# Performance work log

Hardware: AMD Instinct MI355X
Metric: run time of the kernel (lower is better)

The kernel has to match this reference:

```python
import jax, jax.numpy as jnp
import numpy as np

B, SQ, SKV, D = 8, 2048, 2048, 1024

def setup_inputs() -> dict:
    key = jax.random.key(0)
    ks = jax.random.split(key, 8)
    s = 1.0 / np.sqrt(D)  # torch Linear default init range
    return {
        "target": jax.random.normal(ks[0], (B, SQ, D), dtype=jnp.float32),
        "non_target": jax.random.normal(ks[1], (B, SKV, D), dtype=jnp.float32),
        "Wq": jax.random.uniform(ks[2], (D, D), jnp.float32, -s, s),
        "bq": jax.random.uniform(ks[3], (D,), jnp.float32, -s, s),
        "Wk": jax.random.uniform(ks[4], (D, D), jnp.float32, -s, s),
        "bk": jax.random.uniform(ks[5], (D,), jnp.float32, -s, s),
        "Wv": jax.random.uniform(ks[6], (D, D), jnp.float32, -s, s),
        "bv": jax.random.uniform(ks[7], (D,), jnp.float32, -s, s),
    }

def reference(target, non_target, Wq, bq, Wk, bk, Wv, bv):
    # Linear projections (torch Linear: x @ W.T + b)
    q = jnp.einsum('bsd,ed->bse', target, Wq) + bq       # [B,SQ,D]
    k = jnp.einsum('bsd,ed->bse', non_target, Wk) + bk   # [B,SKV,D]
    v = jnp.einsum('bsd,ed->bse', non_target, Wv) + bv   # [B,SKV,D]
    # Unscaled attention, exactly as the original module (no 1/sqrt(d))
    scores = jnp.einsum('bqd,bkd->bqk', q, k)            # [B,SQ,SKV]
    weights = jax.nn.softmax(scores, axis=-1)
    return jnp.einsum('bqk,bkd->bqd', weights, v)        # [B,SQ,D]
```

## Files before the change

kernel.cpp:

```cpp
#include <hip/hip_runtime.h>


typedef _Float16 half8 __attribute__((ext_vector_type(8)));
typedef _Float16 half4v __attribute__((ext_vector_type(4)));
typedef float floatx4 __attribute__((ext_vector_type(4)));

__device__ __forceinline__ void async_copy16(const _Float16* g, _Float16* l) {
  __builtin_amdgcn_global_load_lds(
      (const __attribute__((address_space(1))) void*)g,
      (__attribute__((address_space(3))) void*)l,
      16, 0, 0);
}

__global__ __launch_bounds__(256) void cast_f32_f16(const float* __restrict__ src,
                                                    _Float16* __restrict__ dst, long n) {
  long i = ((long)blockIdx.x * 256 + threadIdx.x) * 8;
  if (i >= n) return;
  float4 a = *(const float4*)(src + i);
  float4 b = *(const float4*)(src + i + 4);
  half8 h;
  h[0] = (_Float16)a.x; h[1] = (_Float16)a.y; h[2] = (_Float16)a.z; h[3] = (_Float16)a.w;
  h[4] = (_Float16)b.x; h[5] = (_Float16)b.y; h[6] = (_Float16)b.z; h[7] = (_Float16)b.w;
  *(half8*)(dst + i) = h;
}

template <int OMODE>
__global__ __launch_bounds__(256, 2) void gemm_bt(const _Float16* __restrict__ A,
                                                  const _Float16* __restrict__ B,
                                                  const float* __restrict__ bias,
                                                  void* __restrict__ out,
                                                  int K, int N,
                                                  long sA, long sB, long sO) {
  __shared__ __attribute__((aligned(16))) _Float16 As[128 * 64];
  __shared__ __attribute__((aligned(16))) _Float16 Bs[128 * 64];

  const int tid = threadIdx.x;
  const int lane = tid & 63;
  const int wave = tid >> 6;
  const long bz = blockIdx.z;

  const _Float16* Ab = A + bz * sA + (long)blockIdx.x * 128 * K;
  const _Float16* Bb = B + bz * sB + (long)blockIdx.y * 128 * K;

  const int wm = (wave & 1) * 64;
  const int wn = (wave >> 1) * 64;
  const int frow = lane & 15;
  const int fq = lane >> 4;
  const int fsw = frow & 7;

  floatx4 acc[4][4];
#pragma unroll
  for (int mt = 0; mt < 4; mt++)
#pragma unroll
    for (int nt = 0; nt < 4; nt++)
      acc[mt][nt] = (floatx4){0.f, 0.f, 0.f, 0.f};

  const int sr = tid >> 3;
  const int gl = (tid & 7) ^ (sr & 7);
  const long gOffBase = (long)sr * K + gl * 8;
  const int ldsOff = tid * 8;

  for (int k0 = 0; k0 < K; k0 += 64) {
    __syncthreads();
#pragma unroll
    for (int j = 0; j < 4; j++) {
      async_copy16(Ab + gOffBase + (long)(32 * j) * K + k0, As + ldsOff + j * 2048);
      async_copy16(Bb + gOffBase + (long)(32 * j) * K + k0, Bs + ldsOff + j * 2048);
    }
    __syncthreads();

#pragma unroll
    for (int h = 0; h < 2; h++) {
      half8 af[4], bf[4];
#pragma unroll
      for (int mt = 0; mt < 4; mt++)
        af[mt] = *(const half8*)(As + (wm + mt * 16 + frow) * 64 + ((h * 4 + fq) ^ fsw) * 8);
#pragma unroll
      for (int nt = 0; nt < 4; nt++)
        bf[nt] = *(const half8*)(Bs + (wn + nt * 16 + frow) * 64 + ((h * 4 + fq) ^ fsw) * 8);
#pragma unroll
      for (int mt = 0; mt < 4; mt++)
#pragma unroll
        for (int nt = 0; nt < 4; nt++)
          acc[mt][nt] = __builtin_amdgcn_mfma_f32_16x16x32_f16(af[mt], bf[nt], acc[mt][nt], 0, 0, 0);
    }
  }

  if (OMODE == 2 || OMODE == 3) {
#pragma unroll
    for (int nt = 0; nt < 4; nt++) {
      const int n = blockIdx.y * 128 + wn + nt * 16 + frow;
#pragma unroll
      for (int mt = 0; mt < 4; mt++) {
        const int rbase = blockIdx.x * 128 + wm + mt * 16 + fq * 4;
#pragma unroll
        for (int i = 0; i < 4; i++) {
          if (OMODE == 2)
            ((float*)out + bz * sO)[(long)(rbase + i) * N + n] = acc[mt][nt][i];
          else
            ((_Float16*)out + bz * sO)[(long)(rbase + i) * N + n] = (_Float16)acc[mt][nt][i];
        }
      }
    }
  } else {
#pragma unroll
    for (int nt = 0; nt < 4; nt++) {
      const int n = blockIdx.y * 128 + wn + nt * 16 + frow;
      const float bvv = bias[n];
#pragma unroll
      for (int mt = 0; mt < 4; mt++) {
        const int rbase = blockIdx.x * 128 + wm + mt * 16 + fq * 4;
        if (OMODE == 0) {
#pragma unroll
          for (int i = 0; i < 4; i++)
            ((_Float16*)out)[(long)(rbase + i) * N + n] = (_Float16)(acc[mt][nt][i] + bvv);
        } else {
          const long bb = rbase >> 11;
          const int s = rbase & 2047;
          half4v hv;
#pragma unroll
          for (int i = 0; i < 4; i++) hv[i] = (_Float16)(acc[mt][nt][i] + bvv);
          *(half4v*)((_Float16*)out + bb * (2048l * 1024) + (long)n * 2048 + s) = hv;
        }
      }
    }
  }
}

__global__ __launch_bounds__(256) void softmax_rows(const _Float16* __restrict__ S,
                                                    _Float16* __restrict__ P) {
  const long row = blockIdx.x;
  const _Float16* src = S + row * 2048;
  _Float16* dst = P + row * 2048;
  const int tid = threadIdx.x;

  half8 v = ((const half8*)src)[tid];
  float f[8];
#pragma unroll
  for (int i = 0; i < 8; i++) f[i] = (float)v[i];

  float m = fmaxf(fmaxf(fmaxf(f[0], f[1]), fmaxf(f[2], f[3])),
                  fmaxf(fmaxf(f[4], f[5]), fmaxf(f[6], f[7])));
#pragma unroll
  for (int o = 32; o > 0; o >>= 1) m = fmaxf(m, __shfl_xor(m, o, 64));
  __shared__ float redm[4];
  if ((tid & 63) == 0) redm[tid >> 6] = m;
  __syncthreads();
  m = fmaxf(fmaxf(redm[0], redm[1]), fmaxf(redm[2], redm[3]));

  float e[8], s = 0.f;
#pragma unroll
  for (int i = 0; i < 8; i++) { e[i] = __expf(f[i] - m); s += e[i]; }
#pragma unroll
  for (int o = 32; o > 0; o >>= 1) s += __shfl_xor(s, o, 64);
  __shared__ float reds[4];
  if ((tid & 63) == 0) reds[tid >> 6] = s;
  __syncthreads();
  s = (reds[0] + reds[1]) + (reds[2] + reds[3]);
  const float inv = 1.f / s;

  half8 h;
#pragma unroll
  for (int i = 0; i < 8; i++) h[i] = (_Float16)(e[i] * inv);
  ((half8*)dst)[tid] = h;
}

extern "C" void kernel_launch(void* const* d_in, const int* in_sizes, int n_in,
                              void* d_out, int out_size, void* d_ws, size_t ws_size,
                              hipStream_t stream) {
  const float* target = (const float*)d_in[0];
  const float* non_target = (const float*)d_in[1];
  const float* Wq = (const float*)d_in[2];
  const float* bq = (const float*)d_in[3];
  const float* Wk = (const float*)d_in[4];
  const float* bk = (const float*)d_in[5];
  const float* Wv = (const float*)d_in[6];
  const float* bv = (const float*)d_in[7];

  char* ws = (char*)d_ws;
  const size_t MB = 1ull << 20;
  _Float16* tgt16 = (_Float16*)(ws);
  _Float16* ntg16 = (_Float16*)(ws + 32 * MB);
  _Float16* S16 = (_Float16*)(ws);
  _Float16* P16 = (_Float16*)(ws + 64 * MB);
  _Float16* Q16 = (_Float16*)(ws + 128 * MB);
  _Float16* K16 = (_Float16*)(ws + 160 * MB);
  _Float16* Vt16 = (_Float16*)(ws + 192 * MB);
  _Float16* Wq16 = (_Float16*)(ws + 224 * MB);
  _Float16* Wk16 = (_Float16*)(ws + 226 * MB);
  _Float16* Wv16 = (_Float16*)(ws + 228 * MB);

  const long nBig = 8l * 2048 * 1024;
  const long nW = 1024l * 1024;

  cast_f32_f16<<<8192, 256, 0, stream>>>(target, tgt16, nBig);
  cast_f32_f16<<<8192, 256, 0, stream>>>(non_target, ntg16, nBig);
  cast_f32_f16<<<512, 256, 0, stream>>>(Wq, Wq16, nW);
  cast_f32_f16<<<512, 256, 0, stream>>>(Wk, Wk16, nW);
  cast_f32_f16<<<512, 256, 0, stream>>>(Wv, Wv16, nW);

  gemm_bt<0><<<dim3(128, 8, 1), 256, 0, stream>>>(tgt16, Wq16, bq, Q16, 1024, 1024, 0, 0, 0);
  gemm_bt<0><<<dim3(128, 8, 1), 256, 0, stream>>>(ntg16, Wk16, bk, K16, 1024, 1024, 0, 0, 0);
  gemm_bt<1><<<dim3(128, 8, 1), 256, 0, stream>>>(ntg16, Wv16, bv, Vt16, 1024, 1024, 0, 0, 0);

  gemm_bt<3><<<dim3(16, 16, 8), 256, 0, stream>>>(Q16, K16, nullptr, S16, 1024, 2048,
                                                  2048l * 1024, 2048l * 1024, 2048l * 2048);

  softmax_rows<<<16384, 256, 0, stream>>>(S16, P16);

  gemm_bt<2><<<dim3(16, 8, 8), 256, 0, stream>>>(P16, Vt16, nullptr, (float*)d_out, 2048, 1024,
                                                 2048l * 2048, 1024l * 2048, 2048l * 1024);
}
```

Measured before the change: 479.0 us.

## Replace 128x128 GEMM with 256x256 tile, 4-stage async LDS pipeline

Replaces the GEMM kernel with a 512-thread, 256x256-tile version. It uses a 4-slot ring of 32-wide K chunks in LDS, prefetches three chunks ahead with global_load_lds, and interleaves the A/B prefetches with MFMA phases. Barriers are split, with s_setprio raised around the MFMA blocks. The aim is to hide global load latency and raise arithmetic intensity per block. In exchange it uses 128KB of LDS per block and launches fewer blocks, which can cut occupancy or leave CUs idle on the smaller GEMMs.

Measured after the change: 495.3 us. 3.4% more time.

```diff
diff --git a/kernel.cpp b/kernel.cpp
--- a/kernel.cpp
+++ b/kernel.cpp
@@ -25,102 +25,139 @@
 }
 
 template <int OMODE>
-__global__ __launch_bounds__(256, 2) void gemm_bt(const _Float16* __restrict__ A,
-                                                  const _Float16* __restrict__ B,
+__global__ __launch_bounds__(512, 2) void gemm256(const _Float16* __restrict__ A,
+                                                  const _Float16* __restrict__ Bm,
                                                   const float* __restrict__ bias,
                                                   void* __restrict__ out,
                                                   int K, int N,
                                                   long sA, long sB, long sO) {
-  __shared__ __attribute__((aligned(16))) _Float16 As[128 * 64];
-  __shared__ __attribute__((aligned(16))) _Float16 Bs[128 * 64];
+  __shared__ __attribute__((aligned(16))) _Float16 lds[65536];
+  _Float16* Ar = lds;
+  _Float16* Br = lds + 32768;
 
   const int tid = threadIdx.x;
   const int lane = tid & 63;
   const int wave = tid >> 6;
+  const int wm = wave >> 2;
+  const int wn = wave & 3;
+  const int frow = lane & 15;
+  const int fq = (lane >> 4) & 3;
   const long bz = blockIdx.z;
 
-  const _Float16* Ab = A + bz * sA + (long)blockIdx.x * 128 * K;
-  const _Float16* Bb = B + bz * sB + (long)blockIdx.y * 128 * K;
-
-  const int wm = (wave & 1) * 64;
-  const int wn = (wave >> 1) * 64;
-  const int frow = lane & 15;
-  const int fq = lane >> 4;
-  const int fsw = frow & 7;
-
-  floatx4 acc[4][4];
-#pragma unroll
-  for (int mt = 0; mt < 4; mt++)
-#pragma unroll
-    for (int nt = 0; nt < 4; nt++)
-      acc[mt][nt] = (floatx4){0.f, 0.f, 0.f, 0.f};
-
-  const int sr = tid >> 3;
-  const int gl = (tid & 7) ^ (sr & 7);
-  const long gOffBase = (long)sr * K + gl * 8;
-  const int ldsOff = tid * 8;
-
-  for (int k0 = 0; k0 < K; k0 += 64) {
-    __syncthreads();
-#pragma unroll
-    for (int j = 0; j < 4; j++) {
-      async_copy16(Ab + gOffBase + (long)(32 * j) * K + k0, As + ldsOff + j * 2048);
-      async_copy16(Bb + gOffBase + (long)(32 * j) * K + k0, Bs + ldsOff + j * 2048);
-    }
-    __syncthreads();
-
-#pragma unroll
-    for (int h = 0; h < 2; h++) {
-      half8 af[4], bf[4];
-#pragma unroll
-      for (int mt = 0; mt < 4; mt++)
-        af[mt] = *(const half8*)(As + (wm + mt * 16 + frow) * 64 + ((h * 4 + fq) ^ fsw) * 8);
-#pragma unroll
-      for (int nt = 0; nt < 4; nt++)
-        bf[nt] = *(const half8*)(Bs + (wn + nt * 16 + frow) * 64 + ((h * 4 + fq) ^ fsw) * 8);
-#pragma unroll
-      for (int mt = 0; mt < 4; mt++)
-#pragma unroll
-        for (int nt = 0; nt < 4; nt++)
-          acc[mt][nt] = __builtin_amdgcn_mfma_f32_16x16x32_f16(af[mt], bf[nt], acc[mt][nt], 0, 0, 0);
-    }
+  const _Float16* Ab = A + bz * sA + (long)blockIdx.x * 256 * K;
+  const _Float16* Bb = Bm + bz * sB + (long)blockIdx.y * 256 * K;
+
+  const int glog = (tid & 7) ^ ((tid >> 3) & 7);
+  const long sg = (long)(2 * (tid >> 3) + (glog >> 2)) * K + (glog & 3) * 8;
+  const int ldst = tid * 8;
+  const long lK128 = (long)K * 128;
+
+  const int gphys = ((frow & 1) * 4 + fq) ^ (frow >> 1);
+  const int aoff = (frow >> 1) * 64 + gphys * 8;
+
+  floatx4 acc[8][4];
+#pragma unroll
+  for (int m = 0; m < 8; ++m)
+#pragma unroll
+    for (int n = 0; n < 4; ++n) acc[m][n] = (floatx4){0.f, 0.f, 0.f, 0.f};
+
+  const int NK = K >> 5;
+
+#pragma unroll
+  for (int kp = 0; kp < 3; ++kp) {
+#pragma unroll
+    for (int j = 0; j < 2; ++j)
+      async_copy16(Ab + sg + kp * 32 + j * lK128, Ar + kp * 8192 + ldst + j * 4096);
+#pragma unroll
+    for (int j = 0; j < 2; ++j)
+      async_copy16(Bb + sg + kp * 32 + j * lK128, Br + kp * 8192 + ldst + j * 4096);
   }
-
-  if (OMODE == 2 || OMODE == 3) {
-#pragma unroll
-    for (int nt = 0; nt < 4; nt++) {
-      const int n = blockIdx.y * 128 + wn + nt * 16 + frow;
-#pragma unroll
-      for (int mt = 0; mt < 4; mt++) {
-        const int rbase = blockIdx.x * 128 + wm + mt * 16 + fq * 4;
-#pragma unroll
-        for (int i = 0; i < 4; i++) {
-          if (OMODE == 2)
-            ((float*)out + bz * sO)[(long)(rbase + i) * N + n] = acc[mt][nt][i];
-          else
-            ((_Float16*)out + bz * sO)[(long)(rbase + i) * N + n] = (_Float16)acc[mt][nt][i];
+  asm volatile("s_waitcnt vmcnt(8)" ::: "memory");
+  __builtin_amdgcn_s_barrier();
+
+  for (int kc = 0; kc < NK; ++kc) {
+    const int slot = kc & 3;
+    int ks = kc + 3;
+    if (ks > NK - 1) ks = NK - 1;
+    const int ssl = ks & 3;
+    const _Float16* as = Ar + slot * 8192 + wm * 4096 + aoff;
+    const _Float16* bs = Br + slot * 8192 + wn * 2048 + aoff;
+
+    half8 af[4], bf[4];
+
+#pragma unroll
+    for (int i = 0; i < 4; ++i) af[i] = *(const half8*)(as + i * 512);
+#pragma unroll
+    for (int n = 0; n < 4; ++n) bf[n] = *(const half8*)(bs + n * 512);
+#pragma unroll
+    for (int j = 0; j < 2; ++j)
+      async_copy16(Ab + sg + ks * 32 + j * lK128, Ar + ssl * 8192 + ldst + j * 4096);
+    __builtin_amdgcn_s_barrier();
+    asm volatile("s_waitcnt lgkmcnt(0)" ::: "memory");
+    __builtin_amdgcn_sched_barrier(0);
+    __builtin_amdgcn_s_setprio(1);
+#pragma unroll
+    for (int i = 0; i < 4; ++i)
+#pragma unroll
+      for (int n = 0; n < 4; ++n)
+        acc[i][n] = __builtin_amdgcn_mfma_f32_16x16x32_f16(af[i], bf[n], acc[i][n], 0, 0, 0);
+    __builtin_amdgcn_s_setprio(0);
+    __builtin_amdgcn_s_barrier();
+
+#pragma unroll
+    for (int i = 0; i < 4; ++i) af[i] = *(const half8*)(as + 2048 + i * 512);
+#pragma unroll
+    for (int j = 0; j < 2; ++j)
+      async_copy16(Bb + sg + ks * 32 + j * lK128, Br + ssl * 8192 + ldst + j * 4096);
+    __builtin_amdgcn_s_barrier();
+    asm volatile("s_waitcnt lgkmcnt(0)" ::: "memory");
+    __builtin_amdgcn_sched_barrier(0);
+    __builtin_amdgcn_s_setprio(1);
+#pragma unroll
+    for (int i = 0; i < 4; ++i)
+#pragma unroll
+      for (int n = 0; n < 4; ++n)
+        acc[4 + i][n] = __builtin_amdgcn_mfma_f32_16x16x32_f16(af[i], bf[n], acc[4 + i][n], 0, 0, 0);
+    __builtin_amdgcn_s_setprio(0);
+    asm volatile("s_waitcnt vmcnt(8)" ::: "memory");
+    __builtin_amdgcn_s_barrier();
+  }
+
+  if (OMODE == 0 || OMODE == 1) {
+#pragma unroll
+    for (int n = 0; n < 4; ++n) {
+      const int cg = blockIdx.y * 256 + wn * 64 + n * 16 + frow;
+      const float bvv = bias[cg];
+#pragma unroll
+      for (int m = 0; m < 8; ++m) {
+        const int rg = blockIdx.x * 256 + wm * 128 + m * 16 + fq * 4;
+        if (OMODE == 0) {
+#pragma unroll
+          for (int i = 0; i < 4; ++i)
+            ((_Float16*)out)[(long)(rg + i) * N + cg] = (_Float16)(acc[m][n][i] + bvv);
+        } else {
+          const long bb = rg >> 11;
+          const int s = rg & 2047;
+          half4v hv;
+#pragma unroll
+          for (int i = 0; i < 4; ++i) hv[i] = (_Float16)(acc[m][n][i] + bvv);
+          *(half4v*)((_Float16*)out + bb * (2048l * 1024) + (long)cg * 2048 + s) = hv;
         }
       }
     }
   } else {
 #pragma unroll
-    for (int nt = 0; nt < 4; nt++) {
-      const int n = blockIdx.y * 128 + wn + nt * 16 + frow;
-      const float bvv = bias[n];
-#pragma unroll
-      for (int mt = 0; mt < 4; mt++) {
-        const int rbase = blockIdx.x * 128 + wm + mt * 16 + fq * 4;
-        if (OMODE == 0) {
-#pragma unroll
-          for (int i = 0; i < 4; i++)
-            ((_Float16*)out)[(long)(rbase + i) * N + n] = (_Float16)(acc[mt][nt][i] + bvv);
-        } else {
-          const long bb = rbase >> 11;
-          const int s = rbase & 2047;
-          half4v hv;
-#pragma unroll
-          for (int i = 0; i < 4; i++) hv[i] = (_Float16)(acc[mt][nt][i] + bvv);
-          *(half4v*)((_Float16*)out + bb * (2048l * 1024) + (long)n * 2048 + s) = hv;
+    for (int n = 0; n < 4; ++n) {
+      const int cg = blockIdx.y * 256 + wn * 64 + n * 16 + frow;
+#pragma unroll
+      for (int m = 0; m < 8; ++m) {
+        const int rgl = blockIdx.x * 256 + wm * 128 + m * 16 + fq * 4;
+#pragma unroll
+        for (int i = 0; i < 4; ++i) {
+          if (OMODE == 2)
+            ((float*)out + bz * sO)[(long)(rgl + i) * N + cg] = acc[m][n][i];
+          else
+            ((_Float16*)out + bz * sO)[(long)(rgl + i) * N + cg] = (_Float16)acc[m][n][i];
         }
       }
     }
@@ -199,15 +236,15 @@
   cast_f32_f16<<<512, 256, 0, stream>>>(Wk, Wk16, nW);
   cast_f32_f16<<<512, 256, 0, stream>>>(Wv, Wv16, nW);
 
-  gemm_bt<0><<<dim3(128, 8, 1), 256, 0, stream>>>(tgt16, Wq16, bq, Q16, 1024, 1024, 0, 0, 0);
-  gemm_bt<0><<<dim3(128, 8, 1), 256, 0, stream>>>(ntg16, Wk16, bk, K16, 1024, 1024, 0, 0, 0);
-  gemm_bt<1><<<dim3(128, 8, 1), 256, 0, stream>>>(ntg16, Wv16, bv, Vt16, 1024, 1024, 0, 0, 0);
-
-  gemm_bt<3><<<dim3(16, 16, 8), 256, 0, stream>>>(Q16, K16, nullptr, S16, 1024, 2048,
-                                                  2048l * 1024, 2048l * 1024, 2048l * 2048);
+  gemm256<0><<<dim3(64, 4, 1), 512, 0, stream>>>(tgt16, Wq16, bq, Q16, 1024, 1024, 0, 0, 0);
+  gemm256<0><<<dim3(64, 4, 1), 512, 0, stream>>>(ntg16, Wk16, bk, K16, 1024, 1024, 0, 0, 0);
+  gemm256<1><<<dim3(64, 4, 1), 512, 0, stream>>>(ntg16, Wv16, bv, Vt16, 1024, 1024, 0, 0, 0);
+
+  gemm256<3><<<dim3(8, 8, 8), 512, 0, stream>>>(Q16, K16, nullptr, S16, 1024, 2048,
+                                                2048l * 1024, 2048l * 1024, 2048l * 2048);
 
   softmax_rows<<<16384, 256, 0, stream>>>(S16, P16);
 
-  gemm_bt<2><<<dim3(16, 8, 8), 256, 0, stream>>>(P16, Vt16, nullptr, (float*)d_out, 2048, 1024,
-                                                 2048l * 2048, 1024l * 2048, 2048l * 1024);
-}
+  gemm256<2><<<dim3(8, 4, 8), 512, 0, stream>>>(P16, Vt16, nullptr, (float*)d_out, 2048, 1024,
+                                                2048l * 2048, 1024l * 2048, 2048l * 1024);
+}
```

## Fuse input casts into projection GEMMs and softmax normalization into PV GEMM

Applied to the files above, without the earlier changes.

The projection GEMMs now read fp32 activations directly and convert them to fp16 in registers before the LDS store, so the two large standalone cast kernels and their intermediate buffers go away. The softmax kernel now writes only each row's max and inverse sum, and the PV GEMM applies exp and normalization to the raw scores while loading its A tile, so the probability matrix is never written or read back. The cost is synchronous global loads instead of async LDS copies for the A operand, and exp work repeated for every N-tile block (8 per row block) in the PV GEMM.

Result: slower. 550.4 us (+14.9%).

```diff
diff --git a/kernel.cpp b/kernel.cpp
--- a/kernel.cpp
+++ b/kernel.cpp
@@ -24,10 +24,12 @@
   *(half8*)(dst + i) = h;
 }
 
-template <int OMODE>
-__global__ __launch_bounds__(256, 2) void gemm_bt(const _Float16* __restrict__ A,
+template <int OMODE, int ATRANS>
+__global__ __launch_bounds__(256, 2) void gemm_bt(const void* __restrict__ A,
                                                   const _Float16* __restrict__ B,
                                                   const float* __restrict__ bias,
+                                                  const float* __restrict__ rowM,
+                                                  const float* __restrict__ rowS,
                                                   void* __restrict__ out,
                                                   int K, int N,
                                                   long sA, long sB, long sO) {
@@ -39,7 +41,9 @@
   const int wave = tid >> 6;
   const long bz = blockIdx.z;
 
-  const _Float16* Ab = A + bz * sA + (long)blockIdx.x * 128 * K;
+  const long abase = bz * sA + (long)blockIdx.x * 128 * K;
+  const _Float16* Ah = (const _Float16*)A + abase;
+  const float* Af = (const float*)A + abase;
   const _Float16* Bb = B + bz * sB + (long)blockIdx.y * 128 * K;
 
   const int wm = (wave & 1) * 64;
@@ -60,12 +64,63 @@
   const long gOffBase = (long)sr * K + gl * 8;
   const int ldsOff = tid * 8;
 
+  float mA0 = 0.f, sA0 = 0.f, mA1 = 0.f, sA1 = 0.f;
+  float mA2 = 0.f, sA2 = 0.f, mA3 = 0.f, sA3 = 0.f;
+  if (ATRANS == 2) {
+    const long gr = bz * 2048 + (long)blockIdx.x * 128 + sr;
+    mA0 = rowM[gr];      sA0 = rowS[gr];
+    mA1 = rowM[gr + 32]; sA1 = rowS[gr + 32];
+    mA2 = rowM[gr + 64]; sA2 = rowS[gr + 64];
+    mA3 = rowM[gr + 96]; sA3 = rowS[gr + 96];
+  }
+
   for (int k0 = 0; k0 < K; k0 += 64) {
     __syncthreads();
-#pragma unroll
-    for (int j = 0; j < 4; j++) {
-      async_copy16(Ab + gOffBase + (long)(32 * j) * K + k0, As + ldsOff + j * 2048);
-      async_copy16(Bb + gOffBase + (long)(32 * j) * K + k0, Bs + ldsOff + j * 2048);
+    if (ATRANS == 0) {
+#pragma unroll
+      for (int j = 0; j < 4; j++) {
+        async_copy16(Ah + gOffBase + (long)(32 * j) * K + k0, As + ldsOff + j * 2048);
+        async_copy16(Bb + gOffBase + (long)(32 * j) * K + k0, Bs + ldsOff + j * 2048);
+      }
+    } else if (ATRANS == 1) {
+      floatx4 f0[4], f1[4];
+#pragma unroll
+      for (int j = 0; j < 4; j++) {
+        const float* src = Af + gOffBase + (long)(32 * j) * K + k0;
+        f0[j] = *(const floatx4*)(src);
+        f1[j] = *(const floatx4*)(src + 4);
+      }
+#pragma unroll
+      for (int j = 0; j < 4; j++)
+        async_copy16(Bb + gOffBase + (long)(32 * j) * K + k0, Bs + ldsOff + j * 2048);
+#pragma unroll
+      for (int j = 0; j < 4; j++) {
+        half8 w;
+#pragma unroll
+        for (int t = 0; t < 4; t++) {
+          w[t] = (_Float16)f0[j][t];
+          w[4 + t] = (_Float16)f1[j][t];
+        }
+        *(half8*)(As + ldsOff + j * 2048) = w;
+      }
+    } else {
+      half8 hv[4];
+#pragma unroll
+      for (int j = 0; j < 4; j++)
+        hv[j] = *(const half8*)(Ah + gOffBase + (long)(32 * j) * K + k0);
+#pragma unroll
+      for (int j = 0; j < 4; j++)
+        async_copy16(Bb + gOffBase + (long)(32 * j) * K + k0, Bs + ldsOff + j * 2048);
+#pragma unroll
+      for (int j = 0; j < 4; j++) {
+        const float mj = (j == 0) ? mA0 : (j == 1) ? mA1 : (j == 2) ? mA2 : mA3;
+        const float sj = (j == 0) ? sA0 : (j == 1) ? sA1 : (j == 2) ? sA2 : sA3;
+        half8 w;
+#pragma unroll
+        for (int t = 0; t < 8; t++)
+          w[t] = (_Float16)(__expf((float)hv[j][t] - mj) * sj);
+        *(half8*)(As + ldsOff + j * 2048) = w;
+      }
     }
     __syncthreads();
 
@@ -127,11 +182,11 @@
   }
 }
 
-__global__ __launch_bounds__(256) void softmax_rows(const _Float16* __restrict__ S,
-                                                    _Float16* __restrict__ P) {
+__global__ __launch_bounds__(256) void rowstat(const _Float16* __restrict__ S,
+                                               float* __restrict__ rowM,
+                                               float* __restrict__ rowS) {
   const long row = blockIdx.x;
   const _Float16* src = S + row * 2048;
-  _Float16* dst = P + row * 2048;
   const int tid = threadIdx.x;
 
   half8 v = ((const half8*)src)[tid];
@@ -148,21 +203,20 @@
   __syncthreads();
   m = fmaxf(fmaxf(redm[0], redm[1]), fmaxf(redm[2], redm[3]));
 
-  float e[8], s = 0.f;
-#pragma unroll
-  for (int i = 0; i < 8; i++) { e[i] = __expf(f[i] - m); s += e[i]; }
+  float s = 0.f;
+#pragma unroll
+  for (int i = 0; i < 8; i++) s += __expf(f[i] - m);
 #pragma unroll
   for (int o = 32; o > 0; o >>= 1) s += __shfl_xor(s, o, 64);
   __shared__ float reds[4];
   if ((tid & 63) == 0) reds[tid >> 6] = s;
   __syncthreads();
   s = (reds[0] + reds[1]) + (reds[2] + reds[3]);
-  const float inv = 1.f / s;
-
-  half8 h;
-#pragma unroll
-  for (int i = 0; i < 8; i++) h[i] = (_Float16)(e[i] * inv);
-  ((half8*)dst)[tid] = h;
+
+  if (tid == 0) {
+    rowM[row] = m;
+    rowS[row] = 1.f / s;
+  }
 }
 
 extern "C" void kernel_launch(void* const* d_in, const int* in_sizes, int n_in,
@@ -179,10 +233,9 @@
 
   char* ws = (char*)d_ws;
   const size_t MB = 1ull << 20;
-  _Float16* tgt16 = (_Float16*)(ws);
-  _Float16* ntg16 = (_Float16*)(ws + 32 * MB);
   _Float16* S16 = (_Float16*)(ws);
-  _Float16* P16 = (_Float16*)(ws + 64 * MB);
+  float* mrow = (float*)(ws + 64 * MB);
+  float* srow = (float*)(ws + 65 * MB);
   _Float16* Q16 = (_Float16*)(ws + 128 * MB);
   _Float16* K16 = (_Float16*)(ws + 160 * MB);
   _Float16* Vt16 = (_Float16*)(ws + 192 * MB);
@@ -190,24 +243,26 @@
   _Float16* Wk16 = (_Float16*)(ws + 226 * MB);
   _Float16* Wv16 = (_Float16*)(ws + 228 * MB);
 
-  const long nBig = 8l * 2048 * 1024;
   const long nW = 1024l * 1024;
 
-  cast_f32_f16<<<8192, 256, 0, stream>>>(target, tgt16, nBig);
-  cast_f32_f16<<<8192, 256, 0, stream>>>(non_target, ntg16, nBig);
   cast_f32_f16<<<512, 256, 0, stream>>>(Wq, Wq16, nW);
   cast_f32_f16<<<512, 256, 0, stream>>>(Wk, Wk16, nW);
   cast_f32_f16<<<512, 256, 0, stream>>>(Wv, Wv16, nW);
 
-  gemm_bt<0><<<dim3(128, 8, 1), 256, 0, stream>>>(tgt16, Wq16, bq, Q16, 1024, 1024, 0, 0, 0);
-  gemm_bt<0><<<dim3(128, 8, 1), 256, 0, stream>>>(ntg16, Wk16, bk, K16, 1024, 1024, 0, 0, 0);
-  gemm_bt<1><<<dim3(128, 8, 1), 256, 0, stream>>>(ntg16, Wv16, bv, Vt16, 1024, 1024, 0, 0, 0);
-
-  gemm_bt<3><<<dim3(16, 16, 8), 256, 0, stream>>>(Q16, K16, nullptr, S16, 1024, 2048,
-                                                  2048l * 1024, 2048l * 1024, 2048l * 2048);
-
-  softmax_rows<<<16384, 256, 0, stream>>>(S16, P16);
-
-  gemm_bt<2><<<dim3(16, 8, 8), 256, 0, stream>>>(P16, Vt16, nullptr, (float*)d_out, 2048, 1024,
-                                                 2048l * 2048, 1024l * 2048, 2048l * 1024);
-}
+  gemm_bt<0, 1><<<dim3(128, 8, 1), 256, 0, stream>>>(target, Wq16, bq, nullptr, nullptr,
+                                                     Q16, 1024, 1024, 0, 0, 0);
+  gemm_bt<0, 1><<<dim3(128, 8, 1), 256, 0, stream>>>(non_target, Wk16, bk, nullptr, nullptr,
+                                                     K16, 1024, 1024, 0, 0, 0);
+  gemm_bt<1, 1><<<dim3(128, 8, 1), 256, 0, stream>>>(non_target, Wv16, bv, nullptr, nullptr,
+                                                     Vt16, 1024, 1024, 0, 0, 0);
+
+  gemm_bt<3, 0><<<dim3(16, 16, 8), 256, 0, stream>>>(Q16, K16, nullptr, nullptr, nullptr,
+                                                     S16, 1024, 2048,
+                                                     2048l * 1024, 2048l * 1024, 2048l * 2048);
+
+  rowstat<<<16384, 256, 0, stream>>>(S16, mrow, srow);
+
+  gemm_bt<2, 2><<<dim3(16, 8, 8), 256, 0, stream>>>(S16, Vt16, nullptr, mrow, srow,
+                                                    (float*)d_out, 2048, 1024,
+                                                    2048l * 2048, 1024l * 2048, 2048l * 1024);
+}
```

## Merge casts and QKV projections into single launches, add tile swizzle for L2 reuse

Applied to the files above, without the earlier changes.

The five cast launches become one kernel that picks its source and destination by block index. The three Q/K/V projection GEMMs become one launch with blockIdx.z selecting the matrix and bias, relying on the 16 MB workspace spacing between tgt16/ntg16, Wq/Wk/Wv and Q/K/Vt. Block-index swizzles are added to the QK^T and PV GEMMs so blocks running together share A/B tiles in L2. This removes launch overhead and tail effects and may improve cache hit rates, at the cost of depending on fixed workspace offsets.

Result: faster. 465.7 us (-2.8%).

```diff
diff --git a/kernel.cpp b/kernel.cpp
--- a/kernel.cpp
+++ b/kernel.cpp
@@ -12,22 +12,40 @@
       16, 0, 0);
 }
 
-__global__ __launch_bounds__(256) void cast_f32_f16(const float* __restrict__ src,
-                                                    _Float16* __restrict__ dst, long n) {
-  long i = ((long)blockIdx.x * 256 + threadIdx.x) * 8;
-  if (i >= n) return;
+__global__ __launch_bounds__(256) void cast_all(const float* __restrict__ t,
+                                                const float* __restrict__ nt,
+                                                const float* __restrict__ wq,
+                                                const float* __restrict__ wk,
+                                                const float* __restrict__ wv,
+                                                _Float16* __restrict__ tgt16,
+                                                _Float16* __restrict__ ntg16,
+                                                _Float16* __restrict__ wq16,
+                                                _Float16* __restrict__ wk16,
+                                                _Float16* __restrict__ wv16) {
+  const int b = blockIdx.x;
+  const float* src;
+  _Float16* dst;
+  long base;
+  if (b < 8192)       { src = t;  dst = tgt16; base = (long)b * 2048; }
+  else if (b < 16384) { src = nt; dst = ntg16; base = (long)(b - 8192) * 2048; }
+  else if (b < 16896) { src = wq; dst = wq16;  base = (long)(b - 16384) * 2048; }
+  else if (b < 17408) { src = wk; dst = wk16;  base = (long)(b - 16896) * 2048; }
+  else                { src = wv; dst = wv16;  base = (long)(b - 17408) * 2048; }
+  const long i = base + (long)threadIdx.x * 8;
   float4 a = *(const float4*)(src + i);
-  float4 b = *(const float4*)(src + i + 4);
+  float4 c = *(const float4*)(src + i + 4);
   half8 h;
   h[0] = (_Float16)a.x; h[1] = (_Float16)a.y; h[2] = (_Float16)a.z; h[3] = (_Float16)a.w;
-  h[4] = (_Float16)b.x; h[5] = (_Float16)b.y; h[6] = (_Float16)b.z; h[7] = (_Float16)b.w;
+  h[4] = (_Float16)c.x; h[5] = (_Float16)c.y; h[6] = (_Float16)c.z; h[7] = (_Float16)c.w;
   *(half8*)(dst + i) = h;
 }
 
-template <int OMODE>
+template <int OMODE, int SWZ>
 __global__ __launch_bounds__(256, 2) void gemm_bt(const _Float16* __restrict__ A,
                                                   const _Float16* __restrict__ B,
                                                   const float* __restrict__ bias,
+                                                  const float* __restrict__ biasK,
+                                                  const float* __restrict__ biasV,
                                                   void* __restrict__ out,
                                                   int K, int N,
                                                   long sA, long sB, long sO) {
@@ -39,8 +57,20 @@
   const int wave = tid >> 6;
   const long bz = blockIdx.z;
 
-  const _Float16* Ab = A + bz * sA + (long)blockIdx.x * 128 * K;
-  const _Float16* Bb = B + bz * sB + (long)blockIdx.y * 128 * K;
+  int bx = blockIdx.x, by = blockIdx.y;
+  if (SWZ == 1) {
+    const int h = bx + 16 * by, g = h & 7, idx = h >> 3;
+    bx = (g & 3) * 4 + (idx & 3);
+    by = (g >> 2) * 8 + (idx >> 2);
+  } else if (SWZ == 2) {
+    const int h = bx + 16 * by, g = h & 7, idx = h >> 3;
+    bx = (g & 3) * 4 + (idx & 3);
+    by = (g >> 2) * 4 + (idx >> 2);
+  }
+
+  const long abase = (OMODE == 4 ? (bz ? sA : 0) : bz * sA) + (long)bx * 128 * K;
+  const _Float16* Ab = A + abase;
+  const _Float16* Bb = B + bz * sB + (long)by * 128 * K;
 
   const int wm = (wave & 1) * 64;
   const int wn = (wave >> 1) * 64;
@@ -89,10 +119,10 @@
   if (OMODE == 2 || OMODE == 3) {
 #pragma unroll
     for (int nt = 0; nt < 4; nt++) {
-      const int n = blockIdx.y * 128 + wn + nt * 16 + frow;
+      const int n = by * 128 + wn + nt * 16 + frow;
 #pragma unroll
       for (int mt = 0; mt < 4; mt++) {
-        const int rbase = blockIdx.x * 128 + wm + mt * 16 + fq * 4;
+        const int rbase = bx * 128 + wm + mt * 16 + fq * 4;
 #pragma unroll
         for (int i = 0; i < 4; i++) {
           if (OMODE == 2)
@@ -103,24 +133,27 @@
       }
     }
   } else {
+    const float* bp = (bz == 0) ? bias : (bz == 1) ? biasK : biasV;
 #pragma unroll
     for (int nt = 0; nt < 4; nt++) {
-      const int n = blockIdx.y * 128 + wn + nt * 16 + frow;
-      const float bvv = bias[n];
+      const int n = by * 128 + wn + nt * 16 + frow;
+      const float bvv = bp[n];
 #pragma unroll
       for (int mt = 0; mt < 4; mt++) {
-        const int rbase = blockIdx.x * 128 + wm + mt * 16 + fq * 4;
-        if (OMODE == 0) {
+        const int rbase = bx * 128 + wm + mt * 16 + fq * 4;
+        if (bz < 2) {
+          _Float16* o16 = (_Float16*)out + bz * sO;
 #pragma unroll
           for (int i = 0; i < 4; i++)
-            ((_Float16*)out)[(long)(rbase + i) * N + n] = (_Float16)(acc[mt][nt][i] + bvv);
+            o16[(long)(rbase + i) * N + n] = (_Float16)(acc[mt][nt][i] + bvv);
         } else {
+          _Float16* vt = (_Float16*)out + 2 * sO;
           const long bb = rbase >> 11;
           const int s = rbase & 2047;
           half4v hv;
 #pragma unroll
           for (int i = 0; i < 4; i++) hv[i] = (_Float16)(acc[mt][nt][i] + bvv);
-          *(half4v*)((_Float16*)out + bb * (2048l * 1024) + (long)n * 2048 + s) = hv;
+          *(half4v*)(vt + bb * (2048l * 1024) + (long)n * 2048 + s) = hv;
         }
       }
     }
@@ -185,29 +218,25 @@
   _Float16* P16 = (_Float16*)(ws + 64 * MB);
   _Float16* Q16 = (_Float16*)(ws + 128 * MB);
   _Float16* K16 = (_Float16*)(ws + 160 * MB);
-  _Float16* Vt16 = (_Float16*)(ws + 192 * MB);
   _Float16* Wq16 = (_Float16*)(ws + 224 * MB);
   _Float16* Wk16 = (_Float16*)(ws + 226 * MB);
   _Float16* Wv16 = (_Float16*)(ws + 228 * MB);
-
-  const long nBig = 8l * 2048 * 1024;
-  const long nW = 1024l * 1024;
-
-  cast_f32_f16<<<8192, 256, 0, stream>>>(target, tgt16, nBig);
-  cast_f32_f16<<<8192, 256, 0, stream>>>(non_target, ntg16, nBig);
-  cast_f32_f16<<<512, 256, 0, stream>>>(Wq, Wq16, nW);
-  cast_f32_f16<<<512, 256, 0, stream>>>(Wk, Wk16, nW);
-  cast_f32_f16<<<512, 256, 0, stream>>>(Wv, Wv16, nW);
-
-  gemm_bt<0><<<dim3(128, 8, 1), 256, 0, stream>>>(tgt16, Wq16, bq, Q16, 1024, 1024, 0, 0, 0);
-  gemm_bt<0><<<dim3(128, 8, 1), 256, 0, stream>>>(ntg16, Wk16, bk, K16, 1024, 1024, 0, 0, 0);
-  gemm_bt<1><<<dim3(128, 8, 1), 256, 0, stream>>>(ntg16, Wv16, bv, Vt16, 1024, 1024, 0, 0, 0);
-
-  gemm_bt<3><<<dim3(16, 16, 8), 256, 0, stream>>>(Q16, K16, nullptr, S16, 1024, 2048,
-                                                  2048l * 1024, 2048l * 1024, 2048l * 2048);
+  _Float16* Vt16 = (_Float16*)(ws + 192 * MB);
+
+  cast_all<<<17920, 256, 0, stream>>>(target, non_target, Wq, Wk, Wv,
+                                      tgt16, ntg16, Wq16, Wk16, Wv16);
+
+  gemm_bt<4, 0><<<dim3(128, 8, 3), 256, 0, stream>>>(
+      tgt16, Wq16, bq, bk, bv, Q16, 1024, 1024,
+      16777216l, 1048576l, 16777216l);
+
+  gemm_bt<3, 1><<<dim3(16, 16, 8), 256, 0, stream>>>(
+      Q16, K16, nullptr, nullptr, nullptr, S16, 1024, 2048,
+      2048l * 1024, 2048l * 1024, 2048l * 2048);
 
   softmax_rows<<<16384, 256, 0, stream>>>(S16, P16);
 
-  gemm_bt<2><<<dim3(16, 8, 8), 256, 0, stream>>>(P16, Vt16, nullptr, (float*)d_out, 2048, 1024,
-                                                 2048l * 2048, 1024l * 2048, 2048l * 1024);
-}
+  gemm_bt<2, 2><<<dim3(16, 8, 8), 256, 0, stream>>>(
+      P16, Vt16, nullptr, nullptr, nullptr, (float*)d_out, 2048, 1024,
+      2048l * 2048, 1024l * 2048, 2048l * 1024);
+}
```
